# Kernel optimization log

Hardware: AMD Instinct MI355X
Metric: run time of the kernel (lower is better)

## Reference

```python
import jax, jax.numpy as jnp
import numpy as np
import itertools as it

K = 10          # delay taps
SKIP = 2        # stride between taps
TRANSIENTS = 100
P = 3           # monomial degree

# monomial index table: all degree-P combinations_with_replacement of the K linear features
_MONOM_IDX = jnp.asarray(list(it.combinations_with_replacement(range(K), P)), dtype=jnp.int32)  # [nlin_dim, P]


def setup_inputs() -> dict:
    key = jax.random.key(0)
    X = jax.random.normal(key, (8, 4, 4096), dtype=jnp.float32)  # [batch, row, n_steps]
    return {"X": X}


def reference(X):
    # X: [b, r, n]; n_dim = 1 after the original unsqueeze(3)
    b, r, n = X.shape
    pad = (K - 1) * SKIP
    # zero-padded delay embedding replaces the roll loop:
    # lin_features[b,r,i,j] = X[b,r, i - (K-1-j)*SKIP], zero for negative time
    Xpad = jnp.pad(X, ((0, 0), (0, 0), (pad, 0)))           # [b, r, n+pad]
    idx = jnp.arange(n)[:, None] + jnp.arange(K)[None, :] * SKIP  # [n, K]
    lin_features = Xpad[:, :, idx]                          # [b, r, n, K]
    # monomial (degree-P) features: gather then product over the small P axis
    nlin_features = jnp.prod(lin_features[..., _MONOM_IDX], axis=-1)  # [b, r, n, nlin_dim]
    tot = jnp.concatenate([lin_features, nlin_features], axis=3)[:, :, TRANSIENTS:, :]
    ones = jnp.ones(tot.shape[:3] + (1,), dtype=tot.dtype)  # bias column
    return jnp.concatenate([ones, tot], axis=3)             # [b, r, n-TRANSIENTS, 1+K+nlin_dim]
```

## Files before the change

kernel.cpp:

```cpp
#include <hip/hip_runtime.h>

#define KTAPS 10
#define SKIP  2
#define TRANS 100
#define PAD   ((KTAPS - 1) * SKIP)
#define NMONO 220
#define NFEAT 231
#define NIN   4096
#define NT    (NIN - TRANS)
#define NROWS 32
#define TT    64
#define RS    233

__global__ __launch_bounds__(256) void nvar_kernel(const float* __restrict__ X,
                                                   float* __restrict__ out) {
    __shared__ float feat[TT * RS];

    const int tile = blockIdx.x;
    const int row  = blockIdx.y;
    const int t0   = tile * TT;
    const int tcount = min(TT, NT - t0);

    const int tl = threadIdx.x & 63;
    const int wq = __builtin_amdgcn_readfirstlane(threadIdx.x >> 6);

    int tg = t0 + tl;
    if (tg >= NT) tg = NT - 1;

    const float* xrow = X + (size_t)row * NIN;
    float tap[KTAPS];
#pragma unroll
    for (int k = 0; k < KTAPS; ++k)
        tap[k] = xrow[tg + (TRANS - PAD) + 2 * k];

    float* frow = feat + tl * RS;

    if (wq == 0) {
        frow[0] = 1.0f;
#pragma unroll
        for (int k = 0; k < KTAPS; ++k)
            frow[1 + k] = tap[k];
    }

    const int plo = (wq == 0) ? 0 : (wq == 1) ? 6 : (wq == 2) ? 19 : 32;
    const int phi = (wq == 0) ? 6 : (wq == 1) ? 19 : (wq == 2) ? 32 : 55;

    {
        int p = 0, fbase = 1 + KTAPS;
#pragma unroll
        for (int i = 0; i < KTAPS; ++i) {
#pragma unroll
            for (int j = i; j < KTAPS; ++j) {
                if (p >= plo && p < phi) {
                    const float pij = tap[i] * tap[j];
#pragma unroll
                    for (int l = j; l < KTAPS; ++l)
                        frow[fbase + (l - j)] = pij * tap[l];
                }
                fbase += KTAPS - j;
                ++p;
            }
        }
    }

    __syncthreads();

    const int total2 = (tcount * NFEAT) >> 1;
    float* obase = out + ((size_t)row * NT + t0) * NFEAT;
    for (int e2 = threadIdx.x; e2 < total2; e2 += 256) {
        const int e0 = e2 << 1;
        const int t  = (unsigned)e0 / NFEAT;
        const int f  = e0 - t * NFEAT;
        const int base = t * RS + f;
        const float a0 = feat[base];
        const float a1 = feat[base + 1 + ((f + 1 >= NFEAT) ? (RS - NFEAT) : 0)];
        reinterpret_cast<float2*>(obase)[e2] = make_float2(a0, a1);
    }
}

extern "C" void kernel_launch(void* const* d_in, const int* in_sizes, int n_in,
                              void* d_out, int out_size, void* d_ws, size_t ws_size,
                              hipStream_t stream) {
    const float* X = (const float*)d_in[0];
    float* out = (float*)d_out;
    dim3 grid((NT + TT - 1) / TT, NROWS);
    nvar_kernel<<<grid, 256, 0, stream>>>(X, out);
}
```

Baseline: 125.0 us.

## Use packed shared tile with float4 copy-out, smaller tiles, templated monomial split

Shared-memory rows are now packed at stride 231 instead of a padded stride. This makes the whole time tile one contiguous block that can be streamed to global memory with float4 loads and stores, replacing the float2 path with its per-element division. The time tile shrinks to 32 and launch bounds request more resident blocks. The per-wave monomial ranges become compile-time template instantiations. In exchange, the two 32-lane halves of each wave compute duplicate feature rows, so half of the compute threads do redundant work.

```diff
diff --git a/kernel.cpp b/kernel.cpp
--- a/kernel.cpp
+++ b/kernel.cpp
@@ -4,25 +4,48 @@
 #define SKIP  2
 #define TRANS 100
 #define PAD   ((KTAPS - 1) * SKIP)
-#define NMONO 220
 #define NFEAT 231
 #define NIN   4096
 #define NT    (NIN - TRANS)
 #define NROWS 32
-#define TT    64
-#define RS    233
+#define TT    32
 
-__global__ __launch_bounds__(256) void nvar_kernel(const float* __restrict__ X,
-                                                   float* __restrict__ out) {
-    __shared__ float feat[TT * RS];
+template<int PLO, int PHI, bool LIN>
+__device__ __forceinline__ void emit_features(const float* __restrict__ tap,
+                                              float* __restrict__ frow) {
+    if (LIN) {
+        frow[0] = 1.0f;
+#pragma unroll
+        for (int k = 0; k < KTAPS; ++k) frow[1 + k] = tap[k];
+    }
+    int p = 0, fb = 1 + KTAPS;
+#pragma unroll
+    for (int i = 0; i < KTAPS; ++i) {
+#pragma unroll
+        for (int j = i; j < KTAPS; ++j) {
+            if (p >= PLO && p < PHI) {
+                const float pij = tap[i] * tap[j];
+#pragma unroll
+                for (int l = j; l < KTAPS; ++l)
+                    frow[fb + (l - j)] = pij * tap[l];
+            }
+            fb += KTAPS - j;
+            ++p;
+        }
+    }
+}
+
+__global__ __launch_bounds__(256, 5) void nvar_kernel(const float* __restrict__ X,
+                                                      float* __restrict__ out) {
+    __shared__ float feat[TT * NFEAT];
 
     const int tile = blockIdx.x;
     const int row  = blockIdx.y;
     const int t0   = tile * TT;
     const int tcount = min(TT, NT - t0);
 
-    const int tl = threadIdx.x & 63;
-    const int wq = __builtin_amdgcn_readfirstlane(threadIdx.x >> 6);
+    const int tl = threadIdx.x & 31;
+    const int wq = threadIdx.x >> 6;
 
     int tg = t0 + tl;
     if (tg >= NT) tg = NT - 1;
@@ -33,49 +56,22 @@
     for (int k = 0; k < KTAPS; ++k)
         tap[k] = xrow[tg + (TRANS - PAD) + 2 * k];
 
-    float* frow = feat + tl * RS;
-
-    if (wq == 0) {
-        frow[0] = 1.0f;
-#pragma unroll
-        for (int k = 0; k < KTAPS; ++k)
-            frow[1 + k] = tap[k];
-    }
-
-    const int plo = (wq == 0) ? 0 : (wq == 1) ? 6 : (wq == 2) ? 19 : 32;
-    const int phi = (wq == 0) ? 6 : (wq == 1) ? 19 : (wq == 2) ? 32 : 55;
-
-    {
-        int p = 0, fbase = 1 + KTAPS;
-#pragma unroll
-        for (int i = 0; i < KTAPS; ++i) {
-#pragma unroll
-            for (int j = i; j < KTAPS; ++j) {
-                if (p >= plo && p < phi) {
-                    const float pij = tap[i] * tap[j];
-#pragma unroll
-                    for (int l = j; l < KTAPS; ++l)
-                        frow[fbase + (l - j)] = pij * tap[l];
-                }
-                fbase += KTAPS - j;
-                ++p;
-            }
-        }
+    float* frow = feat + tl * NFEAT;
+    switch (wq) {
+        case 0:  emit_features< 0,  6, true >(tap, frow); break;
+        case 1:  emit_features< 6, 19, false>(tap, frow); break;
+        case 2:  emit_features<19, 31, false>(tap, frow); break;
+        default: emit_features<31, 55, false>(tap, frow); break;
     }
 
     __syncthreads();
 
-    const int total2 = (tcount * NFEAT) >> 1;
-    float* obase = out + ((size_t)row * NT + t0) * NFEAT;
-    for (int e2 = threadIdx.x; e2 < total2; e2 += 256) {
-        const int e0 = e2 << 1;
-        const int t  = (unsigned)e0 / NFEAT;
-        const int f  = e0 - t * NFEAT;
-        const int base = t * RS + f;
-        const float a0 = feat[base];
-        const float a1 = feat[base + 1 + ((f + 1 >= NFEAT) ? (RS - NFEAT) : 0)];
-        reinterpret_cast<float2*>(obase)[e2] = make_float2(a0, a1);
-    }
+    const int total4 = (tcount * NFEAT) >> 2;
+    float4* __restrict__ o4 =
+        reinterpret_cast<float4*>(out + ((size_t)row * NT + t0) * NFEAT);
+    const float4* s4 = reinterpret_cast<const float4*>(feat);
+    for (int i = threadIdx.x; i < total4; i += 256)
+        o4[i] = s4[i];
 }
 
 extern "C" void kernel_launch(void* const* d_in, const int* in_sizes, int n_in,
```

Result: faster. 121.3 us (-2.9%).
